# Kernel optimization log

Measured on AMD Instinct MI355X. Metric: run time of the kernel, lower is better.

Reference implementation:

```python
import jax, jax.numpy as jnp
import numpy as np

B, S, D, H = 2, 2048, 1024, 16
HD = D // H          # head_dim = 64
HALF = HD // 2       # rotary pair count = 32


def rope_freqs(seq_len, half, base=10000.0):
    # Llama-style: theta_j = base^(-2j/head_dim), angle m*theta_j
    inv = 1.0 / (base ** (np.arange(0, half, dtype=np.float32) / half))
    ang = np.arange(seq_len, dtype=np.float32)[:, None] * inv[None, :]  # [S, half]
    return jnp.asarray(np.cos(ang)), jnp.asarray(np.sin(ang))


def setup_inputs() -> dict:
    key = jax.random.key(0)
    kx, kq, kk, kv, ko = jax.random.split(key, 5)
    cos, sin = rope_freqs(S, HALF)  # real/imag of m_theta_polar_tensor
    s = 0.02
    return {
        "x": jax.random.normal(kx, (B, S, D), dtype=jnp.float32),
        "freqs_cos": cos,
        "freqs_sin": sin,
        "Wq": jax.random.normal(kq, (D, D), dtype=jnp.float32) * s,
        "Wk": jax.random.normal(kk, (D, D), dtype=jnp.float32) * s,
        "Wv": jax.random.normal(kv, (D, D), dtype=jnp.float32) * s,
        "Wout": jax.random.normal(ko, (D, D), dtype=jnp.float32) * s,
    }


def _apply_rope(t, cos, sin):
    # t: [B, S, H, HD]; rotate consecutive pairs (complex multiply)
    b, s, h, hd = t.shape
    tr = t.reshape(b, s, h, hd // 2, 2)
    t0, t1 = tr[..., 0], tr[..., 1]
    c = cos[None, :, None, :]  # [1, S, 1, HALF]
    sn = sin[None, :, None, :]
    o0 = t0 * c - t1 * sn
    o1 = t0 * sn + t1 * c
    return jnp.stack([o0, o1], axis=-1).reshape(b, s, h, hd)


def reference(x, freqs_cos, freqs_sin, Wq, Wk, Wv, Wout):
    b, s, _ = x.shape
    q = (x @ Wq).reshape(b, s, H, HD)
    k = (x @ Wk).reshape(b, s, H, HD)
    v = (x @ Wv).reshape(b, s, H, HD)
    q = _apply_rope(q, freqs_cos, freqs_sin)
    k = _apply_rope(k, freqs_cos, freqs_sin)
    # [B, H, S, S]
    scores = jnp.einsum("bqhd,bkhd->bhqk", q, k) / jnp.sqrt(jnp.float32(HD))
    causal = jnp.triu(jnp.ones((s, s), dtype=bool), k=1)
    scores = jnp.where(causal[None, None], -jnp.inf, scores)
    weights = jax.nn.softmax(scores, axis=-1)
    vectors = jnp.einsum("bhqk,bkhd->bqhd", weights, v).reshape(b, s, D)
    return vectors @ Wout
```

## Files before the change

kernel.cpp:

```cpp
#include <hip/hip_runtime.h>
#include <stdint.h>

typedef unsigned short u16;
typedef __attribute__((ext_vector_type(8))) short short8;
typedef __attribute__((ext_vector_type(4))) float f32x4;
typedef __attribute__((ext_vector_type(4))) unsigned short ushort4v;
typedef __attribute__((ext_vector_type(2))) unsigned int uint2v;

#define NB 2
#define NS 2048
#define ND 1024
#define NH 16
#define HDIM 64
#define NHALF 32
#define QSCALE 0.18033688f
#define NEGBIG -3.0e38f

__device__ __forceinline__ float bf2f(u16 u) {
  union { unsigned u; float f; } v; v.u = ((unsigned)u) << 16; return v.f;
}
__device__ __forceinline__ u16 f2bf(float f) {
  union { float f; unsigned u; } v; v.f = f;
  unsigned r = v.u + 0x7fffu + ((v.u >> 16) & 1u);
  return (u16)(r >> 16);
}

__device__ __forceinline__ unsigned cvt_pk_bf16(float lo, float hi) {
  unsigned r;
  asm("v_cvt_pk_bf16_f32 %0, %1, %2" : "=v"(r) : "v"(lo), "v"(hi));
  return r;
}

__device__ __forceinline__ void gld_lds16(const u16* g, u16* l) {
  void* gv = (void*)g;
  __builtin_amdgcn_global_load_lds((__attribute__((address_space(1))) void*)gv,
                                   (__attribute__((address_space(3))) void*)l, 16, 0, 0);
}

__global__ void prep(const float* __restrict__ x, u16* __restrict__ xb,
                     const float* __restrict__ W0, const float* __restrict__ W1,
                     const float* __restrict__ W2, const float* __restrict__ W3,
                     u16* __restrict__ dqkv, u16* __restrict__ dout) {
  __shared__ float tile[32][33];
  const int bid = blockIdx.x;
  if (bid < 4096) {
    int i = bid * 256 + threadIdx.x;
    float4 v = ((const float4*)x)[i];
    ushort4v o;
    o.x = f2bf(v.x); o.y = f2bf(v.y); o.z = f2bf(v.z); o.w = f2bf(v.w);
    ((ushort4v*)xb)[i] = o;
  } else {
    int idx = bid - 4096;
    const int z = idx >> 10;
    idx &= 1023;
    const int bx = idx & 31, by = idx >> 5;
    const float* W = (z == 0) ? W0 : (z == 1) ? W1 : (z == 2) ? W2 : W3;
    u16* dst = (z < 3) ? (dqkv + (size_t)z * ND * ND) : dout;
    const int n0 = bx * 32, k0 = by * 32;
    const int tx = threadIdx.x & 31, ty = threadIdx.x >> 5;
#pragma unroll
    for (int i = 0; i < 4; ++i)
      tile[ty + i * 8][tx] = W[(size_t)(k0 + ty + i * 8) * ND + n0 + tx];
    __syncthreads();
#pragma unroll
    for (int i = 0; i < 4; ++i)
      dst[(size_t)(n0 + ty + i * 8) * ND + k0 + tx] = f2bf(tile[tx][ty + i * 8]);
  }
}

template<int MI, int MODE>
__global__ __launch_bounds__(256) void gemm64(
    const u16* __restrict__ A, const u16* __restrict__ BT,
    u16* __restrict__ qo, u16* __restrict__ ko, u16* __restrict__ vo,
    float* __restrict__ fo,
    const float* __restrict__ cosT, const float* __restrict__ sinT) {
  __shared__ u16 smem[2][MI * 2048 + 8192];
  const int tid = threadIdx.x;
  const int w = tid >> 6, lane = tid & 63;
  const int lr = lane & 15, lg = lane >> 4;
  const int bm = blockIdx.y * (MI * 32), bn = blockIdx.x << 7;
  const int wr = (w >> 1) * (MI * 16), wc = (w & 1) << 6;
  f32x4 acc[MI][4] = {};

  const int arow = tid >> 3;
  const int aslot = (tid & 7) ^ (arow & 7);
  const u16* ags = A + (size_t)(bm + arow) * ND + (aslot << 3);
  const u16* bgs = BT + (size_t)(bn + arow) * ND + (aslot << 3);

  int af_off[MI][2], bf_off[4][2];
#pragma unroll
  for (int mi = 0; mi < MI; ++mi)
#pragma unroll
    for (int kk = 0; kk < 2; ++kk)
      af_off[mi][kk] = (wr + mi * 16 + lr) * 64 + ((((kk << 2) + lg) ^ (lr & 7)) << 3);
#pragma unroll
  for (int ni = 0; ni < 4; ++ni)
#pragma unroll
    for (int kk = 0; kk < 2; ++kk)
      bf_off[ni][kk] = (wc + ni * 16 + lr) * 64 + ((((kk << 2) + lg) ^ (lr & 7)) << 3);

#define GSTAGE(BUF, KT)                                                     \
  {                                                                         \
    _Pragma("unroll")                                                       \
    for (int it = 0; it < MI; ++it)                                         \
      gld_lds16(ags + it * (32 * ND) + (KT), &smem[BUF][it * 2048 + w * 512]); \
    _Pragma("unroll")                                                       \
    for (int it = 0; it < 4; ++it)                                          \
      gld_lds16(bgs + it * (32 * ND) + (KT), &smem[BUF][MI * 2048 + it * 2048 + w * 512]); \
  }

  GSTAGE(0, 0);
  __syncthreads();
  int cur = 0;
  for (int kt = 0; kt < ND; kt += 64) {
    if (kt + 64 < ND) GSTAGE(cur ^ 1, kt + 64);
    const u16* As = smem[cur];
    const u16* Bs = smem[cur] + MI * 2048;
#pragma unroll
    for (int kk = 0; kk < 2; ++kk) {
      short8 af[MI], bfr[4];
#pragma unroll
      for (int mi = 0; mi < MI; ++mi)
        af[mi] = *(const short8*)(As + af_off[mi][kk]);
#pragma unroll
      for (int ni = 0; ni < 4; ++ni)
        bfr[ni] = *(const short8*)(Bs + bf_off[ni][kk]);
#pragma unroll
      for (int mi = 0; mi < MI; ++mi)
#pragma unroll
        for (int ni = 0; ni < 4; ++ni) {
          if (MODE == 0)
            acc[mi][ni] = __builtin_amdgcn_mfma_f32_16x16x32_bf16(bfr[ni], af[mi], acc[mi][ni], 0, 0, 0);
          else
            acc[mi][ni] = __builtin_amdgcn_mfma_f32_16x16x32_bf16(af[mi], bfr[ni], acc[mi][ni], 0, 0, 0);
        }
    }
    __syncthreads();
    cur ^= 1;
  }

  if (MODE == 0) {
#pragma unroll
    for (int mi = 0; mi < MI; ++mi) {
      const int m = bm + wr + mi * 16 + lr;
      const int b = m >> 11, s = m & 2047;
      const float* cbase = cosT + s * NHALF;
      const float* sbase = sinT + s * NHALF;
#pragma unroll
      for (int ni = 0; ni < 4; ++ni) {
        const int n = bn + wc + ni * 16 + (lg << 2);
        const int which = n >> 10, hh = (n >> 6) & 15, d0 = n & 63;
        u16* dst = which == 0 ? qo : ko;
        const float sc = which == 0 ? QSCALE : 1.0f;
        const float2 cp = *(const float2*)(cbase + (d0 >> 1));
        const float2 sp = *(const float2*)(sbase + (d0 >> 1));
        const float v0 = acc[mi][ni][0], v1 = acc[mi][ni][1];
        const float v2 = acc[mi][ni][2], v3 = acc[mi][ni][3];
        uint2v pk;
        pk.x = cvt_pk_bf16((v0 * cp.x - v1 * sp.x) * sc, (v0 * sp.x + v1 * cp.x) * sc);
        pk.y = cvt_pk_bf16((v2 * cp.y - v3 * sp.y) * sc, (v2 * sp.y + v3 * cp.y) * sc);
        *(uint2v*)(dst + (((size_t)(b * NH + hh) * NS + s) << 6) + d0) = pk;
      }
    }
  } else if (MODE == 1) {
#pragma unroll
    for (int mi = 0; mi < MI; ++mi) {
#pragma unroll
      for (int ni = 0; ni < 4; ++ni) {
        const int n = bn + wc + ni * 16 + lr;
        const int hh = n >> 6, d = n & 63;
        const int m0 = bm + wr + mi * 16 + (lg << 2);
        const int b = m0 >> 11, s0 = m0 & 2047;
        uint2v pk;
        pk.x = cvt_pk_bf16(acc[mi][ni][0], acc[mi][ni][1]);
        pk.y = cvt_pk_bf16(acc[mi][ni][2], acc[mi][ni][3]);
        *(uint2v*)(vo + ((size_t)(b * NH + hh) * HDIM + d) * NS + s0) = pk;
      }
    }
  } else {
#pragma unroll
    for (int mi = 0; mi < MI; ++mi)
#pragma unroll
      for (int ni = 0; ni < 4; ++ni)
#pragma unroll
        for (int j = 0; j < 4; ++j) {
          const int m = bm + wr + mi * 16 + (lg << 2) + j;
          const int n = bn + wc + ni * 16 + lr;
          fo[(size_t)m * ND + n] = acc[mi][ni][j];
        }
  }
}

__global__ __launch_bounds__(256, 4) void attn_k(
    const u16* __restrict__ Qb, const u16* __restrict__ Kb,
    const u16* __restrict__ VT, u16* __restrict__ Ob) {
  __shared__ u16 K2[2][4096];
  __shared__ u16 V2[2][4096];
  __shared__ u16 Pl[4][1024];
  const int tid = threadIdx.x, w = tid >> 6, lane = tid & 63;
  const int lr = lane & 15, lg = lane >> 4;
  const int bid = blockIdx.x;
  const int xcd = bid & 7, i = bid >> 3;
  const int bh = xcd * 4 + (i & 3);
  const int pair = i >> 2;
  const int b = bh >> 4, h = bh & 15;
  const u16* Qp = Qb + (size_t)bh * NS * HDIM;
  const u16* Kp = Kb + (size_t)bh * NS * HDIM;
  const u16* Vp = VT + (size_t)bh * NS * HDIM;

  int kf_off[4][2], vb_off[4][2], pw_off[4], pa_off[2];
#pragma unroll
  for (int u = 0; u < 4; ++u) {
    const int kvr = (u << 4) + lr;
#pragma unroll
    for (int c = 0; c < 2; ++c)
      kf_off[u][c] = kvr * 64 + ((((c << 6) + (lg << 4)) ^ ((kvr & 7) << 4)) >> 1);
  }
#pragma unroll
  for (int dn = 0; dn < 4; ++dn) {
    const int d = (dn << 4) + lr;
#pragma unroll
    for (int ks = 0; ks < 2; ++ks)
      vb_off[dn][ks] = d * 64 + ((((ks << 6) + (lg << 4)) ^ ((d & 7) << 4)) >> 1);
  }
#pragma unroll
  for (int u = 0; u < 4; ++u)
    pw_off[u] = lr * 64 + ((((u << 5) + (lg << 3)) ^ ((lr & 7) << 4)) >> 1);
#pragma unroll
  for (int ks = 0; ks < 2; ++ks)
    pa_off[ks] = lr * 64 + ((((ks << 6) + (lg << 4)) ^ ((lr & 7) << 4)) >> 1);
  u16* Pw = &Pl[w][0];

  const int rr = tid >> 3, slot = tid & 7;
  const int soff = (((slot << 4) ^ ((rr & 7) << 4)) >> 1);
  const u16* kg0 = Kp + rr * HDIM + soff;
  const u16* kg1 = Kp + (rr + 32) * HDIM + soff;
  const u16* vg0 = Vp + (size_t)rr * NS + soff;
  const u16* vg1 = Vp + (size_t)(rr + 32) * NS + soff;

#define STAGE(BUFI, KV0)                                         \
  {                                                              \
    gld_lds16(kg0 + (KV0) * HDIM, &K2[BUFI][w * 512]);           \
    gld_lds16(kg1 + (KV0) * HDIM, &K2[BUFI][(4 + w) * 512]);     \
    gld_lds16(vg0 + (KV0),        &V2[BUFI][w * 512]);           \
    gld_lds16(vg1 + (KV0),        &V2[BUFI][(4 + w) * 512]);     \
  }

#define STEP(BUF, KVT)                                                            \
  {                                                                               \
    const int kv0 = (KVT) << 6;                                                   \
    if ((KVT) + 1 < nst) STAGE(BUF ^ 1, kv0 + 64);                                \
    const u16* Kl = K2[BUF];                                                      \
    const u16* Vl = V2[BUF];                                                      \
    f32x4 st[4] = {};                                                             \
    __builtin_amdgcn_s_setprio(1);                                                \
    _Pragma("unroll") for (int u = 0; u < 4; ++u)                                 \
      _Pragma("unroll") for (int c = 0; c < 2; ++c)                               \
        st[u] = __builtin_amdgcn_mfma_f32_16x16x32_bf16(                          \
            *(const short8*)(Kl + kf_off[u][c]), qf[c], st[u], 0, 0, 0);          \
    __builtin_amdgcn_s_setprio(0);                                                \
    if (kv0 + 63 > qw) {                                                          \
      _Pragma("unroll") for (int u = 0; u < 4; ++u)                               \
        _Pragma("unroll") for (int j = 0; j < 4; ++j) {                           \
          const int kvg = kv0 + (u << 4) + (lg << 2) + j;                         \
          if (kvg > q_col) st[u][j] = NEGBIG;                                     \
        }                                                                         \
    }                                                                             \
    _Pragma("unroll") for (int u = 0; u < 4; ++u) {                               \
      const float e0 = __builtin_amdgcn_exp2f(st[u][0]);                          \
      const float e1 = __builtin_amdgcn_exp2f(st[u][1]);                          \
      const float e2 = __builtin_amdgcn_exp2f(st[u][2]);                          \
      const float e3 = __builtin_amdgcn_exp2f(st[u][3]);                          \
      lacc += (e0 + e1) + (e2 + e3);                                              \
      uint2v pk;                                                                  \
      pk.x = cvt_pk_bf16(e0, e1);                                                 \
      pk.y = cvt_pk_bf16(e2, e3);                                                 \
      *(uint2v*)(Pw + pw_off[u]) = pk;                                            \
    }                                                                             \
    {                                                                             \
      short8 pa0 = *(const short8*)(Pw + pa_off[0]);                              \
      short8 pa1 = *(const short8*)(Pw + pa_off[1]);                              \
      __builtin_amdgcn_s_setprio(1);                                              \
      _Pragma("unroll") for (int dn = 0; dn < 4; ++dn) {                          \
        o[dn] = __builtin_amdgcn_mfma_f32_16x16x32_bf16(                          \
            pa0, *(const short8*)(Vl + vb_off[dn][0]), o[dn], 0, 0, 0);           \
        o[dn] = __builtin_amdgcn_mfma_f32_16x16x32_bf16(                          \
            pa1, *(const short8*)(Vl + vb_off[dn][1]), o[dn], 0, 0, 0);           \
      }                                                                           \
      __builtin_amdgcn_s_setprio(0);                                              \
    }                                                                             \
    __syncthreads();                                                              \
  }

  for (int seg = 0; seg < 2; ++seg) {
    const int tile = seg ? pair : 31 - pair;
    const int q0 = tile << 6;
    const int qw = q0 + w * 16;
    const int q_col = qw + lr;
    const int nst = tile + 1;

    short8 qf[2];
#pragma unroll
    for (int c = 0; c < 2; ++c)
      qf[c] = *(const short8*)(Qp + (size_t)(qw + lr) * HDIM + c * 32 + lg * 8);

    f32x4 o[4] = {};
    float lacc = 0.f;

    STAGE(0, 0);
    __syncthreads();

    int kvt = 0;
    for (; kvt + 2 <= nst; kvt += 2) {
      STEP(0, kvt);
      STEP(1, kvt + 1);
    }
    if (kvt < nst) STEP(0, kvt);

    float rs = lacc;
    rs += __shfl_xor(rs, 16);
    rs += __shfl_xor(rs, 32);
    float li[4];
#pragma unroll
    for (int j = 0; j < 4; ++j) li[j] = 1.0f / __shfl(rs, (lg << 2) + j);
#pragma unroll
    for (int dn = 0; dn < 4; ++dn)
#pragma unroll
      for (int j = 0; j < 4; ++j) {
        const int m = b * NS + qw + (lg << 2) + j;
        const int col = h * 64 + dn * 16 + lr;
        Ob[(size_t)m * ND + col] = f2bf(o[dn][j] * li[j]);
      }
  }
}

extern "C" void kernel_launch(void* const* d_in, const int* in_sizes, int n_in,
                              void* d_out, int out_size, void* d_ws, size_t ws_size,
                              hipStream_t stream) {
  const float* x  = (const float*)d_in[0];
  const float* fc = (const float*)d_in[1];
  const float* fs = (const float*)d_in[2];
  const float* Wq = (const float*)d_in[3];
  const float* Wk = (const float*)d_in[4];
  const float* Wv = (const float*)d_in[5];
  const float* Wo = (const float*)d_in[6];
  float* out = (float*)d_out;
  char* ws = (char*)d_ws;

  u16* xb    = (u16*)(ws);
  u16* Ob    = (u16*)(ws);
  u16* WTqkv = (u16*)(ws + (size_t)(8u << 20));
  u16* WTo   = (u16*)(ws + (size_t)(14u << 20));
  u16* Qb    = (u16*)(ws + (size_t)(16u << 20));
  u16* Kb    = (u16*)(ws + (size_t)(24u << 20));
  u16* VT    = (u16*)(ws + (size_t)(32u << 20));
  u16* WTv   = WTqkv + (size_t)2 * ND * ND;

  prep<<<8192, 256, 0, stream>>>(x, xb, Wq, Wk, Wv, Wo, WTqkv, WTo);
  gemm64<4, 0><<<dim3(16, 32), 256, 0, stream>>>(xb, WTqkv, Qb, Kb, nullptr, nullptr, fc, fs);
  gemm64<2, 1><<<dim3(8, 64), 256, 0, stream>>>(xb, WTv, nullptr, nullptr, VT, nullptr, nullptr, nullptr);
  attn_k<<<512, 256, 0, stream>>>(Qb, Kb, VT, Ob);
  gemm64<2, 2><<<dim3(8, 64), 256, 0, stream>>>(Ob, WTo, nullptr, nullptr, nullptr, out, nullptr, nullptr);
}
```

Baseline: 102.1 us.

## Merge QKV and V projection launches; use 128-row query tiles in attention

The Q/K projection GEMM and the V projection GEMM now run in one kernel launch, with block index ranges picking the variant. This removes a launch boundary and lets both sets of blocks share the GPU at once. The attention kernel moves to 512 threads per block with 8 waves, each block handling a 128-row query tile, so every staged K/V tile is reused by twice as many query rows. In exchange the attention grid drops to 256 blocks and causal masking wastes more work on the larger diagonal tiles, which may reduce occupancy and load balance.

```diff
diff --git a/kernel.cpp b/kernel.cpp
--- a/kernel.cpp
+++ b/kernel.cpp
@@ -69,16 +69,17 @@
 }
 
 template<int MI, int MODE>
-__global__ __launch_bounds__(256) void gemm64(
+__device__ __forceinline__ void gemm_body(
+    u16* smem0, int bx, int by,
     const u16* __restrict__ A, const u16* __restrict__ BT,
     u16* __restrict__ qo, u16* __restrict__ ko, u16* __restrict__ vo,
     float* __restrict__ fo,
     const float* __restrict__ cosT, const float* __restrict__ sinT) {
-  __shared__ u16 smem[2][MI * 2048 + 8192];
+  constexpr int BUFSZ = MI * 2048 + 8192;
   const int tid = threadIdx.x;
   const int w = tid >> 6, lane = tid & 63;
   const int lr = lane & 15, lg = lane >> 4;
-  const int bm = blockIdx.y * (MI * 32), bn = blockIdx.x << 7;
+  const int bm = by * (MI * 32), bn = bx << 7;
   const int wr = (w >> 1) * (MI * 16), wc = (w & 1) << 6;
   f32x4 acc[MI][4] = {};
 
@@ -99,23 +100,23 @@
     for (int kk = 0; kk < 2; ++kk)
       bf_off[ni][kk] = (wc + ni * 16 + lr) * 64 + ((((kk << 2) + lg) ^ (lr & 7)) << 3);
 
-#define GSTAGE(BUF, KT)                                                     \
-  {                                                                         \
-    _Pragma("unroll")                                                       \
-    for (int it = 0; it < MI; ++it)                                         \
-      gld_lds16(ags + it * (32 * ND) + (KT), &smem[BUF][it * 2048 + w * 512]); \
-    _Pragma("unroll")                                                       \
-    for (int it = 0; it < 4; ++it)                                          \
-      gld_lds16(bgs + it * (32 * ND) + (KT), &smem[BUF][MI * 2048 + it * 2048 + w * 512]); \
-  }
-
-  GSTAGE(0, 0);
+  auto stage = [&](int buf, int kt) {
+    u16* dst = smem0 + buf * BUFSZ;
+#pragma unroll
+    for (int it = 0; it < MI; ++it)
+      gld_lds16(ags + it * (32 * ND) + kt, dst + it * 2048 + w * 512);
+#pragma unroll
+    for (int it = 0; it < 4; ++it)
+      gld_lds16(bgs + it * (32 * ND) + kt, dst + MI * 2048 + it * 2048 + w * 512);
+  };
+
+  stage(0, 0);
   __syncthreads();
   int cur = 0;
   for (int kt = 0; kt < ND; kt += 64) {
-    if (kt + 64 < ND) GSTAGE(cur ^ 1, kt + 64);
-    const u16* As = smem[cur];
-    const u16* Bs = smem[cur] + MI * 2048;
+    if (kt + 64 < ND) stage(cur ^ 1, kt + 64);
+    const u16* As = smem0 + cur * BUFSZ;
+    const u16* Bs = As + MI * 2048;
 #pragma unroll
     for (int kk = 0; kk < 2; ++kk) {
       short8 af[MI], bfr[4];
@@ -191,12 +192,32 @@
   }
 }
 
-__global__ __launch_bounds__(256, 4) void attn_k(
+__global__ __launch_bounds__(256) void gemm_qkv(
+    const u16* __restrict__ xb, const u16* __restrict__ WTqkv, const u16* __restrict__ WTv,
+    u16* __restrict__ Qb, u16* __restrict__ Kb, u16* __restrict__ VT,
+    const float* __restrict__ fc, const float* __restrict__ fs) {
+  __shared__ u16 smem[2 * 16384];
+  const int bid = blockIdx.x;
+  if (bid < 512) {
+    gemm_body<4, 0>(smem, bid & 15, bid >> 4, xb, WTqkv, Qb, Kb, nullptr, nullptr, fc, fs);
+  } else {
+    const int idx = bid - 512;
+    gemm_body<2, 1>(smem, idx & 7, idx >> 3, xb, WTv, nullptr, nullptr, VT, nullptr, nullptr, nullptr);
+  }
+}
+
+__global__ __launch_bounds__(256) void gemm_out_k(
+    const u16* __restrict__ Ob, const u16* __restrict__ WTo, float* __restrict__ out) {
+  __shared__ u16 smem[2 * 12288];
+  gemm_body<2, 2>(smem, blockIdx.x, blockIdx.y, Ob, WTo, nullptr, nullptr, nullptr, out, nullptr, nullptr);
+}
+
+__global__ __launch_bounds__(512) void attn_k(
     const u16* __restrict__ Qb, const u16* __restrict__ Kb,
     const u16* __restrict__ VT, u16* __restrict__ Ob) {
   __shared__ u16 K2[2][4096];
   __shared__ u16 V2[2][4096];
-  __shared__ u16 Pl[4][1024];
+  __shared__ u16 Pl[8][1024];
   const int tid = threadIdx.x, w = tid >> 6, lane = tid & 63;
   const int lr = lane & 15, lg = lane >> 4;
   const int bid = blockIdx.x;
@@ -232,18 +253,14 @@
   u16* Pw = &Pl[w][0];
 
   const int rr = tid >> 3, slot = tid & 7;
-  const int soff = (((slot << 4) ^ ((rr & 7) << 4)) >> 1);
-  const u16* kg0 = Kp + rr * HDIM + soff;
-  const u16* kg1 = Kp + (rr + 32) * HDIM + soff;
+  const int soff = ((slot ^ (rr & 7)) << 3);
+  const u16* kg0 = Kp + (size_t)rr * HDIM + soff;
   const u16* vg0 = Vp + (size_t)rr * NS + soff;
-  const u16* vg1 = Vp + (size_t)(rr + 32) * NS + soff;
-
-#define STAGE(BUFI, KV0)                                         \
-  {                                                              \
-    gld_lds16(kg0 + (KV0) * HDIM, &K2[BUFI][w * 512]);           \
-    gld_lds16(kg1 + (KV0) * HDIM, &K2[BUFI][(4 + w) * 512]);     \
-    gld_lds16(vg0 + (KV0),        &V2[BUFI][w * 512]);           \
-    gld_lds16(vg1 + (KV0),        &V2[BUFI][(4 + w) * 512]);     \
+
+#define STAGE(BUFI, KV0)                                   \
+  {                                                        \
+    gld_lds16(kg0 + (size_t)(KV0) * HDIM, &K2[BUFI][w * 512]); \
+    gld_lds16(vg0 + (KV0),                &V2[BUFI][w * 512]); \
   }
 
 #define STEP(BUF, KVT)                                                            \
@@ -293,11 +310,11 @@
   }
 
   for (int seg = 0; seg < 2; ++seg) {
-    const int tile = seg ? pair : 31 - pair;
-    const int q0 = tile << 6;
+    const int tile = seg ? pair : 15 - pair;
+    const int q0 = tile << 7;
     const int qw = q0 + w * 16;
     const int q_col = qw + lr;
-    const int nst = tile + 1;
+    const int nst = 2 * tile + 2;
 
     short8 qf[2];
 #pragma unroll
@@ -310,12 +327,10 @@
     STAGE(0, 0);
     __syncthreads();
 
-    int kvt = 0;
-    for (; kvt + 2 <= nst; kvt += 2) {
+    for (int kvt = 0; kvt < nst; kvt += 2) {
       STEP(0, kvt);
       STEP(1, kvt + 1);
     }
-    if (kvt < nst) STEP(0, kvt);
 
     float rs = lacc;
     rs += __shfl_xor(rs, 16);
@@ -357,8 +372,7 @@
   u16* WTv   = WTqkv + (size_t)2 * ND * ND;
 
   prep<<<8192, 256, 0, stream>>>(x, xb, Wq, Wk, Wv, Wo, WTqkv, WTo);
-  gemm64<4, 0><<<dim3(16, 32), 256, 0, stream>>>(xb, WTqkv, Qb, Kb, nullptr, nullptr, fc, fs);
-  gemm64<2, 1><<<dim3(8, 64), 256, 0, stream>>>(xb, WTv, nullptr, nullptr, VT, nullptr, nullptr, nullptr);
-  attn_k<<<512, 256, 0, stream>>>(Qb, Kb, VT, Ob);
-  gemm64<2, 2><<<dim3(8, 64), 256, 0, stream>>>(Ob, WTo, nullptr, nullptr, nullptr, out, nullptr, nullptr);
-}
+  gemm_qkv<<<1024, 256, 0, stream>>>(xb, WTqkv, WTv, Qb, Kb, VT, fc, fs);
+  attn_k<<<256, 512, 0, stream>>>(Qb, Kb, VT, Ob);
+  gemm_out_k<<<dim3(8, 64), 256, 0, stream>>>(Ob, WTo, out);
+}
```

Measured after the change: 101.9 us. About the same (-0.2%).
